# Kernel optimization log

Measured on AMD Instinct MI355X. Metric: run time of the kernel, lower is better.

The kernel has to match this reference:

```python
import jax, jax.numpy as jnp
import numpy as np

N = 100000
E = 1600000
D_IN = 128
HEADS = 4
C = 16  # hidden // heads
NEG_SLOPE = 0.2


def setup_inputs() -> dict:
    key = jax.random.key(0)
    ks = jax.random.split(key, 8)
    x = jax.random.normal(ks[0], (N, D_IN), dtype=jnp.float32)
    edge_index = jax.random.randint(ks[1], (2, E), 0, N, dtype=jnp.int32)
    s = 1.0 / np.sqrt(D_IN)
    W_l = jax.random.normal(ks[2], (D_IN, HEADS * C), dtype=jnp.float32) * s
    b_l = jnp.zeros((HEADS * C,), dtype=jnp.float32)
    W_r = jax.random.normal(ks[3], (D_IN, HEADS * C), dtype=jnp.float32) * s
    b_r = jnp.zeros((HEADS * C,), dtype=jnp.float32)
    att = jax.random.normal(ks[4], (HEADS, C), dtype=jnp.float32) * (1.0 / np.sqrt(C))
    bias = jnp.zeros((HEADS * C,), dtype=jnp.float32)
    W_head = jax.random.normal(ks[5], (HEADS * C, 1), dtype=jnp.float32) * (1.0 / np.sqrt(HEADS * C))
    b_head = jnp.zeros((1,), dtype=jnp.float32)
    return {"x": x, "edge_index": edge_index, "W_l": W_l, "b_l": b_l,
            "W_r": W_r, "b_r": b_r, "att": att, "bias": bias,
            "W_head": W_head, "b_head": b_head}


def reference(x, edge_index, W_l, b_l, W_r, b_r, att, bias, W_head, b_head):
    # GATv2Conv (PyG semantics, add_self_loops=True, concat=True)
    n = x.shape[0]
    # add self loops
    loops = jnp.arange(n, dtype=edge_index.dtype)
    src = jnp.concatenate([edge_index[0], loops])  # source j
    dst = jnp.concatenate([edge_index[1], loops])  # target i
    # per-node linear projections -> [N, H, C]
    x_l = (x @ W_l + b_l).reshape(n, HEADS, C)
    x_r = (x @ W_r + b_r).reshape(n, HEADS, C)
    # per-edge attention logits: att . LeakyReLU(x_l[j] + x_r[i])
    e = x_l[src] + x_r[dst]                               # [E', H, C]
    e = jnp.where(e >= 0, e, NEG_SLOPE * e)
    logits = jnp.einsum('ehc,hc->eh', e, att)             # [E', H]
    # segment softmax over incoming edges of each target node
    seg_max = jax.ops.segment_max(logits, dst, num_segments=n)  # [N, H]
    expw = jnp.exp(logits - seg_max[dst])
    seg_sum = jax.ops.segment_sum(expw, dst, num_segments=n)
    alpha = expw / seg_sum[dst]                           # [E', H]
    # weighted scatter-aggregate of source messages
    msg = alpha[:, :, None] * x_l[src]                    # [E', H, C]
    out = jax.ops.segment_sum(msg, dst, num_segments=n)   # [N, H, C]
    out = out.reshape(n, HEADS * C) + bias
    # ReLU + Linear head
    h = jax.nn.relu(out)
    return (h @ W_head + b_head).squeeze(-1)              # [N]
```

## Files before the change

### kernel.cpp

```cpp
#include <hip/hip_runtime.h>
#include <hip/hip_bf16.h>
#include <hip/hip_fp16.h>

#define HC 64
#define D_IN 128
#define NEG_SLOPE 0.2f
#define BK 64
#define BKQ 16
#define BCAP2 1536
#define NBIN 2048
#define L2E 1.44269504f

using f32x4 = __attribute__((ext_vector_type(4))) float;
using f16x8 = __attribute__((ext_vector_type(8))) _Float16;
using f16x2 = __attribute__((ext_vector_type(2))) _Float16;

__global__ void k_iota(int* __restrict__ p, int n) {
    int i = blockIdx.x * blockDim.x + threadIdx.x;
    if (i < n) p[i] = i * BCAP2;
}

__global__ __launch_bounds__(256, 3) void k_proj(
    const float* __restrict__ x,
    const float* __restrict__ Wl, const float* __restrict__ bl,
    const float* __restrict__ Wr, const float* __restrict__ br,
    __half* __restrict__ xlh, float* __restrict__ xr, int N) {
    __shared__ _Float16 sWT[128 * 136];
    __shared__ _Float16 sX[32 * 136];
    const int t = threadIdx.x;
    for (int idx = t; idx < 8192; idx += 256) {
        const int k = idx >> 6;
        const int c = idx & 63;
        sWT[c * 136 + k]        = (_Float16)Wl[idx];
        sWT[(c + 64) * 136 + k] = (_Float16)Wr[idx];
    }
    const int lane = t & 63;
    const int wave = t >> 6;
    const int m = lane & 15;
    const int q = lane >> 4;
    float bfu[2];
#pragma unroll
    for (int cc = 0; cc < 2; ++cc) {
        const int ct = wave * 2 + cc;
        const int ch = (ct & 3) * 16 + m;
        bfu[cc] = (ct < 4) ? bl[ch] : br[ch];
    }
    __syncthreads();

    const int ntrip = N >> 5;
    for (int trip = blockIdx.x; trip < ntrip; trip += gridDim.x) {
        const int i0 = trip << 5;
        for (int c = t; c < 1024; c += 256) {
            const int r = c >> 5, c4 = c & 31;
            float4 v = ((const float4*)(x + (size_t)(i0 + r) * D_IN))[c4];
            _Float16* dp = &sX[r * 136 + c4 * 4];
            dp[0] = (_Float16)v.x; dp[1] = (_Float16)v.y;
            dp[2] = (_Float16)v.z; dp[3] = (_Float16)v.w;
        }
        __syncthreads();
        f16x8 af[2][4];
#pragma unroll
        for (int tt = 0; tt < 2; ++tt)
#pragma unroll
            for (int kk = 0; kk < 4; ++kk)
                af[tt][kk] = *(const f16x8*)&sX[(tt * 16 + m) * 136 + kk * 32 + q * 8];
#pragma unroll
        for (int cc = 0; cc < 2; ++cc) {
            const int ct = wave * 2 + cc;
            const _Float16* bp = &sWT[(ct * 16 + m) * 136 + q * 8];
            f32x4 acc0 = {0.f, 0.f, 0.f, 0.f};
            f32x4 acc1 = {0.f, 0.f, 0.f, 0.f};
#pragma unroll
            for (int kk = 0; kk < 4; ++kk) {
                f16x8 bf = *(const f16x8*)(bp + kk * 32);
                acc0 = __builtin_amdgcn_mfma_f32_16x16x32_f16(af[0][kk], bf, acc0, 0, 0, 0);
                acc1 = __builtin_amdgcn_mfma_f32_16x16x32_f16(af[1][kk], bf, acc1, 0, 0, 0);
            }
            const float bv = bfu[cc];
            if (ct < 4) {
                const int ch = ct * 16 + m;
#pragma unroll
                for (int r = 0; r < 4; ++r) {
                    xlh[(size_t)(i0 + q * 4 + r) * HC + ch]      = __float2half(acc0[r] + bv);
                    xlh[(size_t)(i0 + 16 + q * 4 + r) * HC + ch] = __float2half(acc1[r] + bv);
                }
            } else {
                const int ch = (ct - 4) * 16 + m;
#pragma unroll
                for (int r = 0; r < 4; ++r) {
                    xr[(size_t)(i0 + q * 4 + r) * HC + ch]      = acc0[r] + bv;
                    xr[(size_t)(i0 + 16 + q * 4 + r) * HC + ch] = acc1[r] + bv;
                }
            }
        }
        __syncthreads();
    }
}

__global__ __launch_bounds__(256) void k_scat1(const int* __restrict__ src,
                                               const int* __restrict__ dst, int E,
                                               int* __restrict__ bfill,
                                               unsigned* __restrict__ coarse) {
    __shared__ int h[NBIN], bl[NBIN], cur[NBIN];
    const int t = threadIdx.x;
    for (int i = t; i < NBIN; i += 256) { h[i] = 0; cur[i] = 0; }
    __syncthreads();
    const int beg = blockIdx.x * 4096;
    int4 d4[4], s4[4];
#pragma unroll
    for (int r = 0; r < 4; ++r) {
        const int idx = beg + 4 * t + r * 1024;
        if (idx < E) {
            d4[r] = *(const int4*)(dst + idx);
            s4[r] = *(const int4*)(src + idx);
        } else { d4[r] = make_int4(-1, -1, -1, -1); }
    }
#pragma unroll
    for (int r = 0; r < 4; ++r) {
        if (d4[r].x >= 0) {
            atomicAdd(&h[d4[r].x >> 6], 1);
            atomicAdd(&h[d4[r].y >> 6], 1);
            atomicAdd(&h[d4[r].z >> 6], 1);
            atomicAdd(&h[d4[r].w >> 6], 1);
        }
    }
    __syncthreads();
    for (int i = t; i < NBIN; i += 256)
        bl[i] = h[i] ? atomicAdd(&bfill[i], h[i]) : 0;
    __syncthreads();
#pragma unroll
    for (int r = 0; r < 4; ++r) {
        if (d4[r].x >= 0) {
            const int dd[4] = {d4[r].x, d4[r].y, d4[r].z, d4[r].w};
            const int ss[4] = {s4[r].x, s4[r].y, s4[r].z, s4[r].w};
#pragma unroll
            for (int j = 0; j < 4; ++j) {
                const int bin = dd[j] >> 6;
                const int pos = atomicAdd(&cur[bin], 1);
                coarse[bl[bin] + pos] = ((unsigned)ss[j] << 6) | (unsigned)(dd[j] & 63);
            }
        }
    }
}

__device__ __forceinline__ float redpair(float v) {
    int a = __builtin_amdgcn_update_dpp(0, __float_as_int(v), 0xB1, 0xF, 0xF, true);
    return v + __int_as_float(a);
}
__device__ __forceinline__ float red8(float v) {
    int a = __builtin_amdgcn_update_dpp(0, __float_as_int(v), 0x128, 0xF, 0xF, true);
    return v + __int_as_float(a);
}

__global__ __launch_bounds__(256) void k_aggs(
    const __half* __restrict__ xlh, const float* __restrict__ xr,
    const float* __restrict__ att, const float* __restrict__ bias,
    const float* __restrict__ Wh, const float* __restrict__ bh,
    const int* __restrict__ bfill, const unsigned* __restrict__ coarse,
    float* __restrict__ out, int N) {
    __shared__ int s_src[BCAP2];
    __shared__ int s_cnt[BKQ], s_off[BKQ], s_cur[BKQ], s_scan[BKQ];
    const int t = threadIdx.x;
    const int bkt  = blockIdx.x >> 2;
    const int quad = blockIdx.x & 3;
    const int eb = bkt * BCAP2;
    const int ee = bfill[bkt];
    if (t < BKQ) { s_cnt[t] = 0; s_cur[t] = 0; }
    __syncthreads();
    unsigned er[6]; int nr = 0;
#pragma unroll
    for (int r = 0; r < 6; ++r) {
        const int idx = eb + t + r * 256;
        if (idx < ee) {
            const unsigned e = coarse[idx];
            if (((e >> 4) & 3u) == (unsigned)quad) er[nr++] = e;
        }
    }
    for (int k = 0; k < nr; ++k) atomicAdd(&s_cnt[er[k] & 15], 1);
    __syncthreads();
    if (t < BKQ) s_scan[t] = s_cnt[t];
    __syncthreads();
    for (int o = 1; o < BKQ; o <<= 1) {
        int v = (t < BKQ && t >= o) ? s_scan[t - o] : 0;
        __syncthreads();
        if (t < BKQ) s_scan[t] += v;
        __syncthreads();
    }
    if (t < BKQ) s_off[t] = s_scan[t] - s_cnt[t];
    __syncthreads();
    for (int k = 0; k < nr; ++k) {
        const int bin = er[k] & 15;
        const int pos = atomicAdd(&s_cur[bin], 1);
        s_src[s_off[bin] + pos] = (int)(er[k] >> 6);
    }
    __syncthreads();

    const int wave = t >> 6;
    const int lane = t & 63;
    const int sub  = lane & 7;
    const int slot = lane >> 3;
    const _Float16* xlhp = (const _Float16*)xlh;

    const float4 atA = *(const float4*)(att + 8 * sub);
    const float4 atB = *(const float4*)(att + 8 * sub + 4);
    f16x2 at[4];
    at[0][0] = (_Float16)(atA.x * L2E); at[0][1] = (_Float16)(atA.y * L2E);
    at[1][0] = (_Float16)(atA.z * L2E); at[1][1] = (_Float16)(atA.w * L2E);
    at[2][0] = (_Float16)(atB.x * L2E); at[2][1] = (_Float16)(atB.y * L2E);
    at[3][0] = (_Float16)(atB.z * L2E); at[3][1] = (_Float16)(atB.w * L2E);
    const f16x2 c02 = {(_Float16)NEG_SLOPE, (_Float16)NEG_SLOPE};
    const _Float16 h0 = (_Float16)0.f;
    const float4 biA = *(const float4*)(bias + 8 * sub);
    const float4 biB = *(const float4*)(bias + 8 * sub + 4);
    const float4 whA = *(const float4*)(Wh + 8 * sub);
    const float4 whB = *(const float4*)(Wh + 8 * sub + 4);
    const float bhv = bh[0];

    for (int k4 = 0; k4 < 4; ++k4) {
        const int nl = wave + 4 * k4;
        const int i = bkt * 64 + quad * 16 + nl;
        if (i >= N) continue;
        const int beg = s_off[nl];
        const int cnt = s_cnt[nl];

        const float4 xrA = *(const float4*)(xr + ((size_t)i << 6) + 8 * sub);
        const float4 xrB = *(const float4*)(xr + ((size_t)i << 6) + 8 * sub + 4);
        f16x2 xri[4];
        xri[0][0] = (_Float16)xrA.x; xri[0][1] = (_Float16)xrA.y;
        xri[1][0] = (_Float16)xrA.z; xri[1][1] = (_Float16)xrA.w;
        xri[2][0] = (_Float16)xrB.x; xri[2][1] = (_Float16)xrB.y;
        xri[3][0] = (_Float16)xrB.z; xri[3][1] = (_Float16)xrB.w;
        const uint4 xliraw = *(const uint4*)(xlhp + ((size_t)i << 6) + 8 * sub);
        f16x2 xli[4];
        xli[0] = __builtin_bit_cast(f16x2, xliraw.x);
        xli[1] = __builtin_bit_cast(f16x2, xliraw.y);
        xli[2] = __builtin_bit_cast(f16x2, xliraw.z);
        xli[3] = __builtin_bit_cast(f16x2, xliraw.w);

        float t0 = 0.f;
#pragma unroll
        for (int c = 0; c < 4; ++c) {
            f16x2 w = xli[c] + xri[c];
            w = __builtin_elementwise_max(w, w * c02);
            t0 = __builtin_amdgcn_fdot2(at[c], w, t0, false);
        }
        t0 = redpair(t0);
        const _Float16 pe0h = (slot == 0) ? (_Float16)exp2f(t0) : h0;
        const f16x2 p0A = {pe0h, h0};
        const f16x2 p0B = {h0, pe0h};
        float s = (float)pe0h;
        float a[8];
#pragma unroll
        for (int c = 0; c < 4; ++c) {
            a[2 * c]     = __builtin_amdgcn_fdot2(xli[c], p0A, 0.f, false);
            a[2 * c + 1] = __builtin_amdgcn_fdot2(xli[c], p0B, 0.f, false);
        }

        int p = 0;
#define EDGE_GROUP(JEXPR, PRED)                                              \
    {                                                                        \
        const int jj = (JEXPR);                                              \
        const uint4 raw = *(const uint4*)(xlhp + ((size_t)jj << 6) + 8 * sub);\
        f16x2 xv[4];                                                         \
        xv[0] = __builtin_bit_cast(f16x2, raw.x);                            \
        xv[1] = __builtin_bit_cast(f16x2, raw.y);                            \
        xv[2] = __builtin_bit_cast(f16x2, raw.z);                            \
        xv[3] = __builtin_bit_cast(f16x2, raw.w);                            \
        float tt = 0.f;                                                      \
        _Pragma("unroll")                                                    \
        for (int c = 0; c < 4; ++c) {                                        \
            f16x2 w = xv[c] + xri[c];                                        \
            w = __builtin_elementwise_max(w, w * c02);                       \
            tt = __builtin_amdgcn_fdot2(at[c], w, tt, false);                \
        }                                                                    \
        tt = redpair(tt);                                                    \
        const _Float16 peh = (PRED) ? (_Float16)exp2f(tt) : h0;              \
        const f16x2 pA = {peh, h0};                                          \
        const f16x2 pB = {h0, peh};                                          \
        s += (float)peh;                                                     \
        _Pragma("unroll")                                                    \
        for (int c = 0; c < 4; ++c) {                                        \
            a[2 * c]     = __builtin_amdgcn_fdot2(xv[c], pA, a[2 * c], false);\
            a[2 * c + 1] = __builtin_amdgcn_fdot2(xv[c], pB, a[2 * c + 1], false);\
        }                                                                    \
    }
        for (; p + 16 <= cnt; p += 16) {
            const int j0 = s_src[beg + p + slot];
            const int j1 = s_src[beg + p + 8 + slot];
            EDGE_GROUP(j0, true)
            EDGE_GROUP(j1, true)
        }
        if (p + 8 <= cnt) {
            const int j0 = s_src[beg + p + slot];
            EDGE_GROUP(j0, true)
            p += 8;
        }
        const int rem = cnt - p;
        if (rem > 0) {
            const int idx = p + slot;
            const int j0 = s_src[beg + ((idx < cnt) ? idx : (cnt - 1))];
            EDGE_GROUP(j0, slot < rem)
        }
#undef EDGE_GROUP

        s = red8(s);  s += __shfl_xor(s, 16);  s += __shfl_xor(s, 32);
#pragma unroll
        for (int c = 0; c < 8; ++c) {
            a[c] = red8(a[c]);
            a[c] += __shfl_xor(a[c], 16);
            a[c] += __shfl_xor(a[c], 32);
        }
        const float inv = 1.f / s;
        float y = fmaxf(a[0] * inv + biA.x, 0.f) * whA.x
                + fmaxf(a[1] * inv + biA.y, 0.f) * whA.y
                + fmaxf(a[2] * inv + biA.z, 0.f) * whA.z
                + fmaxf(a[3] * inv + biA.w, 0.f) * whA.w
                + fmaxf(a[4] * inv + biB.x, 0.f) * whB.x
                + fmaxf(a[5] * inv + biB.y, 0.f) * whB.y
                + fmaxf(a[6] * inv + biB.z, 0.f) * whB.z
                + fmaxf(a[7] * inv + biB.w, 0.f) * whB.w;
        y += __shfl_xor(y, 1);
        y += __shfl_xor(y, 2);
        y += __shfl_xor(y, 4);
        if (lane == 0) out[i] = y + bhv;
    }
}

extern "C" void kernel_launch(void* const* d_in, const int* in_sizes, int n_in,
                              void* d_out, int out_size, void* d_ws, size_t ws_size,
                              hipStream_t stream) {
    const float* x   = (const float*)d_in[0];
    const int*   ei  = (const int*)d_in[1];
    const float* Wl  = (const float*)d_in[2];
    const float* bl  = (const float*)d_in[3];
    const float* Wr  = (const float*)d_in[4];
    const float* br  = (const float*)d_in[5];
    const float* att = (const float*)d_in[6];
    const float* bias= (const float*)d_in[7];
    const float* Wh  = (const float*)d_in[8];
    const float* bh  = (const float*)d_in[9];
    float* out = (float*)d_out;

    const int N = in_sizes[0] / D_IN;
    const int E = in_sizes[1] / 2;
    const int* src = ei;
    const int* dst = ei + E;
    const int nbkt = (N + BK - 1) / BK;

    auto align = [](size_t v) { return (v + 255) & ~(size_t)255; };
    char* ws = (char*)d_ws;
    size_t off = 0;
    __half* xlh     = (__half*)(ws + off);   off = align(off + (size_t)N * HC * 2);
    float* xr       = (float*)(ws + off);    off = align(off + (size_t)N * HC * 4);
    int*   bfill    = (int*)(ws + off);      off = align(off + NBIN * 4);
    unsigned* coarse= (unsigned*)(ws + off); off = align(off + (size_t)NBIN * BCAP2 * 4);
    (void)ws_size;

    k_iota<<<8, 256, 0, stream>>>(bfill, NBIN);

    k_proj<<<1024, 256, 0, stream>>>(x, Wl, bl, Wr, br, xlh, xr, N);

    k_scat1<<<(E + 4095) / 4096, 256, 0, stream>>>(src, dst, E, bfill, coarse);

    k_aggs<<<nbkt * 4, 256, 0, stream>>>(xlh, xr, att, bias, Wh, bh,
                                         bfill, coarse, out, N);
}
```

Measured before the change: 208.2 us.

## Double-buffer x tiles in projection and shrink scatter blocks, reusing LDS histogram

In the projection kernel, the next tile of x is now prefetched into registers while the current tile is being processed. The shared-memory staging buffer is doubled so one barrier per iteration can be dropped, overlapping global loads with the MFMA work. In the scatter kernel, each block now handles 2048 edges instead of 4096, and the histogram array is zeroed and reused as the per-bin cursor, cutting LDS use and raising block count. The trade-off is more global atomics on the bin fill counters and shorter contiguous runs per bin in the coarse buffer.

```diff
diff --git a/kernel.cpp b/kernel.cpp
--- a/kernel.cpp
+++ b/kernel.cpp
@@ -26,7 +26,7 @@
     const float* __restrict__ Wr, const float* __restrict__ br,
     __half* __restrict__ xlh, float* __restrict__ xr, int N) {
     __shared__ _Float16 sWT[128 * 136];
-    __shared__ _Float16 sX[32 * 136];
+    __shared__ _Float16 sX[2][32 * 136];
     const int t = threadIdx.x;
     for (int idx = t; idx < 8192; idx += 256) {
         const int k = idx >> 6;
@@ -45,25 +45,42 @@
         const int ch = (ct & 3) * 16 + m;
         bfu[cc] = (ct < 4) ? bl[ch] : br[ch];
     }
-    __syncthreads();
 
     const int ntrip = N >> 5;
-    for (int trip = blockIdx.x; trip < ntrip; trip += gridDim.x) {
+    const int rr = t >> 5;
+    const int c4 = t & 31;
+    int trip = blockIdx.x;
+    int tb = 0;
+    float4 xv[4];
+    if (trip < ntrip) {
         const int i0 = trip << 5;
-        for (int c = t; c < 1024; c += 256) {
-            const int r = c >> 5, c4 = c & 31;
-            float4 v = ((const float4*)(x + (size_t)(i0 + r) * D_IN))[c4];
-            _Float16* dp = &sX[r * 136 + c4 * 4];
-            dp[0] = (_Float16)v.x; dp[1] = (_Float16)v.y;
-            dp[2] = (_Float16)v.z; dp[3] = (_Float16)v.w;
+#pragma unroll
+        for (int it = 0; it < 4; ++it)
+            xv[it] = *(const float4*)(x + (size_t)(i0 + rr + 8 * it) * D_IN + c4 * 4);
+    }
+    for (; trip < ntrip; trip += gridDim.x, ++tb) {
+        _Float16* sxb = &sX[tb & 1][0];
+#pragma unroll
+        for (int it = 0; it < 4; ++it) {
+            _Float16* dp = &sxb[(rr + 8 * it) * 136 + c4 * 4];
+            dp[0] = (_Float16)xv[it].x; dp[1] = (_Float16)xv[it].y;
+            dp[2] = (_Float16)xv[it].z; dp[3] = (_Float16)xv[it].w;
         }
         __syncthreads();
+        const int nxt = trip + gridDim.x;
+        if (nxt < ntrip) {
+            const int i0n = nxt << 5;
+#pragma unroll
+            for (int it = 0; it < 4; ++it)
+                xv[it] = *(const float4*)(x + (size_t)(i0n + rr + 8 * it) * D_IN + c4 * 4);
+        }
+        const int i0 = trip << 5;
         f16x8 af[2][4];
 #pragma unroll
         for (int tt = 0; tt < 2; ++tt)
 #pragma unroll
             for (int kk = 0; kk < 4; ++kk)
-                af[tt][kk] = *(const f16x8*)&sX[(tt * 16 + m) * 136 + kk * 32 + q * 8];
+                af[tt][kk] = *(const f16x8*)&sxb[(tt * 16 + m) * 136 + kk * 32 + q * 8];
 #pragma unroll
         for (int cc = 0; cc < 2; ++cc) {
             const int ct = wave * 2 + cc;
@@ -93,7 +110,6 @@
                 }
             }
         }
-        __syncthreads();
     }
 }
 
@@ -101,14 +117,14 @@
                                                const int* __restrict__ dst, int E,
                                                int* __restrict__ bfill,
                                                unsigned* __restrict__ coarse) {
-    __shared__ int h[NBIN], bl[NBIN], cur[NBIN];
+    __shared__ int h[NBIN], bl[NBIN];
     const int t = threadIdx.x;
-    for (int i = t; i < NBIN; i += 256) { h[i] = 0; cur[i] = 0; }
-    __syncthreads();
-    const int beg = blockIdx.x * 4096;
-    int4 d4[4], s4[4];
-#pragma unroll
-    for (int r = 0; r < 4; ++r) {
+    for (int i = t; i < NBIN; i += 256) h[i] = 0;
+    __syncthreads();
+    const int beg = blockIdx.x * 2048;
+    int4 d4[2], s4[2];
+#pragma unroll
+    for (int r = 0; r < 2; ++r) {
         const int idx = beg + 4 * t + r * 1024;
         if (idx < E) {
             d4[r] = *(const int4*)(dst + idx);
@@ -116,7 +132,7 @@
         } else { d4[r] = make_int4(-1, -1, -1, -1); }
     }
 #pragma unroll
-    for (int r = 0; r < 4; ++r) {
+    for (int r = 0; r < 2; ++r) {
         if (d4[r].x >= 0) {
             atomicAdd(&h[d4[r].x >> 6], 1);
             atomicAdd(&h[d4[r].y >> 6], 1);
@@ -125,18 +141,21 @@
         }
     }
     __syncthreads();
-    for (int i = t; i < NBIN; i += 256)
-        bl[i] = h[i] ? atomicAdd(&bfill[i], h[i]) : 0;
-    __syncthreads();
-#pragma unroll
-    for (int r = 0; r < 4; ++r) {
+    for (int i = t; i < NBIN; i += 256) {
+        const int hv = h[i];
+        bl[i] = hv ? atomicAdd(&bfill[i], hv) : 0;
+        h[i] = 0;
+    }
+    __syncthreads();
+#pragma unroll
+    for (int r = 0; r < 2; ++r) {
         if (d4[r].x >= 0) {
             const int dd[4] = {d4[r].x, d4[r].y, d4[r].z, d4[r].w};
             const int ss[4] = {s4[r].x, s4[r].y, s4[r].z, s4[r].w};
 #pragma unroll
             for (int j = 0; j < 4; ++j) {
                 const int bin = dd[j] >> 6;
-                const int pos = atomicAdd(&cur[bin], 1);
+                const int pos = atomicAdd(&h[bin], 1);
                 coarse[bl[bin] + pos] = ((unsigned)ss[j] << 6) | (unsigned)(dd[j] & 63);
             }
         }
@@ -360,7 +379,7 @@
 
     k_proj<<<1024, 256, 0, stream>>>(x, Wl, bl, Wr, br, xlh, xr, N);
 
-    k_scat1<<<(E + 4095) / 4096, 256, 0, stream>>>(src, dst, E, bfill, coarse);
+    k_scat1<<<(E + 2047) / 2048, 256, 0, stream>>>(src, dst, E, bfill, coarse);
 
     k_aggs<<<nbkt * 4, 256, 0, stream>>>(xlh, xr, att, bias, Wh, bh,
                                          bfill, coarse, out, N);
```

New measurement: 215.5 us. 3.5% more time.

## Keep projection weights in registers, load x directly, stage outputs for coalesced stores

Applied to the files above, without the earlier changes.

The projection kernel now keeps each wave's fp16 weight fragments in registers instead of transposing them into shared memory. It loads x straight from global memory into MFMA operand registers, skipping the shared-memory staging pass. Outputs are written to a small shared tile and then stored with coalesced 16-byte writes instead of scattered 2- and 4-byte stores. Occupancy is raised to 4 blocks per SM, at the cost of more register pressure and strided, uncoalesced reads of x and W.

```diff
diff --git a/kernel.cpp b/kernel.cpp
--- a/kernel.cpp
+++ b/kernel.cpp
@@ -20,78 +20,93 @@
     if (i < n) p[i] = i * BCAP2;
 }
 
-__global__ __launch_bounds__(256, 3) void k_proj(
+__global__ __launch_bounds__(256, 4) void k_proj(
     const float* __restrict__ x,
     const float* __restrict__ Wl, const float* __restrict__ bl,
     const float* __restrict__ Wr, const float* __restrict__ br,
     __half* __restrict__ xlh, float* __restrict__ xr, int N) {
-    __shared__ _Float16 sWT[128 * 136];
-    __shared__ _Float16 sX[32 * 136];
+    __shared__ _Float16 sH[32 * 64];
+    __shared__ float    sF[32 * 64];
     const int t = threadIdx.x;
-    for (int idx = t; idx < 8192; idx += 256) {
-        const int k = idx >> 6;
-        const int c = idx & 63;
-        sWT[c * 136 + k]        = (_Float16)Wl[idx];
-        sWT[(c + 64) * 136 + k] = (_Float16)Wr[idx];
-    }
     const int lane = t & 63;
     const int wave = t >> 6;
     const int m = lane & 15;
     const int q = lane >> 4;
+
+    f16x8 bf[2][4];
     float bfu[2];
 #pragma unroll
     for (int cc = 0; cc < 2; ++cc) {
         const int ct = wave * 2 + cc;
         const int ch = (ct & 3) * 16 + m;
+        const float* W = (ct < 4) ? Wl : Wr;
         bfu[cc] = (ct < 4) ? bl[ch] : br[ch];
-    }
-    __syncthreads();
+#pragma unroll
+        for (int kk = 0; kk < 4; ++kk) {
+            const float* wp = W + (size_t)(kk * 32 + q * 8) * 64 + ch;
+            f16x8 v;
+#pragma unroll
+            for (int e = 0; e < 8; ++e)
+                v[e] = (_Float16)wp[(size_t)e * 64];
+            bf[cc][kk] = v;
+        }
+    }
 
     const int ntrip = N >> 5;
     for (int trip = blockIdx.x; trip < ntrip; trip += gridDim.x) {
         const int i0 = trip << 5;
-        for (int c = t; c < 1024; c += 256) {
-            const int r = c >> 5, c4 = c & 31;
-            float4 v = ((const float4*)(x + (size_t)(i0 + r) * D_IN))[c4];
-            _Float16* dp = &sX[r * 136 + c4 * 4];
-            dp[0] = (_Float16)v.x; dp[1] = (_Float16)v.y;
-            dp[2] = (_Float16)v.z; dp[3] = (_Float16)v.w;
-        }
-        __syncthreads();
         f16x8 af[2][4];
 #pragma unroll
-        for (int tt = 0; tt < 2; ++tt)
-#pragma unroll
-            for (int kk = 0; kk < 4; ++kk)
-                af[tt][kk] = *(const f16x8*)&sX[(tt * 16 + m) * 136 + kk * 32 + q * 8];
+        for (int tt = 0; tt < 2; ++tt) {
+            const float* xp = x + (size_t)(i0 + tt * 16 + m) * D_IN + q * 8;
+#pragma unroll
+            for (int kk = 0; kk < 4; ++kk) {
+                const float4 f0 = *(const float4*)(xp + kk * 32);
+                const float4 f1 = *(const float4*)(xp + kk * 32 + 4);
+                f16x8 v;
+                v[0] = (_Float16)f0.x; v[1] = (_Float16)f0.y;
+                v[2] = (_Float16)f0.z; v[3] = (_Float16)f0.w;
+                v[4] = (_Float16)f1.x; v[5] = (_Float16)f1.y;
+                v[6] = (_Float16)f1.z; v[7] = (_Float16)f1.w;
+                af[tt][kk] = v;
+            }
+        }
 #pragma unroll
         for (int cc = 0; cc < 2; ++cc) {
             const int ct = wave * 2 + cc;
-            const _Float16* bp = &sWT[(ct * 16 + m) * 136 + q * 8];
             f32x4 acc0 = {0.f, 0.f, 0.f, 0.f};
             f32x4 acc1 = {0.f, 0.f, 0.f, 0.f};
 #pragma unroll
             for (int kk = 0; kk < 4; ++kk) {
-                f16x8 bf = *(const f16x8*)(bp + kk * 32);
-                acc0 = __builtin_amdgcn_mfma_f32_16x16x32_f16(af[0][kk], bf, acc0, 0, 0, 0);
-                acc1 = __builtin_amdgcn_mfma_f32_16x16x32_f16(af[1][kk], bf, acc1, 0, 0, 0);
+                acc0 = __builtin_amdgcn_mfma_f32_16x16x32_f16(af[0][kk], bf[cc][kk], acc0, 0, 0, 0);
+                acc1 = __builtin_amdgcn_mfma_f32_16x16x32_f16(af[1][kk], bf[cc][kk], acc1, 0, 0, 0);
             }
             const float bv = bfu[cc];
             if (ct < 4) {
                 const int ch = ct * 16 + m;
 #pragma unroll
                 for (int r = 0; r < 4; ++r) {
-                    xlh[(size_t)(i0 + q * 4 + r) * HC + ch]      = __float2half(acc0[r] + bv);
-                    xlh[(size_t)(i0 + 16 + q * 4 + r) * HC + ch] = __float2half(acc1[r] + bv);
+                    sH[(q * 4 + r) * 64 + ch]      = (_Float16)(acc0[r] + bv);
+                    sH[(16 + q * 4 + r) * 64 + ch] = (_Float16)(acc1[r] + bv);
                 }
             } else {
                 const int ch = (ct - 4) * 16 + m;
 #pragma unroll
                 for (int r = 0; r < 4; ++r) {
-                    xr[(size_t)(i0 + q * 4 + r) * HC + ch]      = acc0[r] + bv;
-                    xr[(size_t)(i0 + 16 + q * 4 + r) * HC + ch] = acc1[r] + bv;
+                    sF[(q * 4 + r) * 64 + ch]      = acc0[r] + bv;
+                    sF[(16 + q * 4 + r) * 64 + ch] = acc1[r] + bv;
                 }
             }
+        }
+        __syncthreads();
+        {
+            const uint4* srcH = (const uint4*)sH;
+            uint4* dstH = (uint4*)(xlh + (size_t)i0 * 64);
+            dstH[t] = srcH[t];
+            const uint4* srcF = (const uint4*)sF;
+            uint4* dstF = (uint4*)(xr + (size_t)i0 * 64);
+            dstF[t]       = srcF[t];
+            dstF[t + 256] = srcF[t + 256];
         }
         __syncthreads();
     }
```

After: 212.8 us. +2.2%, slower.

## Merge projection and edge scatter into one launch; store x_r as fp16

Applied to the files above, without the earlier changes.

The projection GEMM and the edge-bucketing scatter now run as one kernel. The first nscat blocks do the scatter and the rest run the projection loop, so the two independent phases overlap and one launch is dropped. x_r is also written as fp16 instead of fp32, which halves its write and read traffic and removes the conversion in the aggregation kernel. The cost is a shared-memory union sized for the larger branch, which may limit occupancy, plus slightly lower precision in the stored x_r.

```diff
diff --git a/kernel.cpp b/kernel.cpp
--- a/kernel.cpp
+++ b/kernel.cpp
@@ -20,14 +20,66 @@
     if (i < n) p[i] = i * BCAP2;
 }
 
-__global__ __launch_bounds__(256, 3) void k_proj(
+__global__ __launch_bounds__(256, 3) void k_projscat(
     const float* __restrict__ x,
     const float* __restrict__ Wl, const float* __restrict__ bl,
     const float* __restrict__ Wr, const float* __restrict__ br,
-    __half* __restrict__ xlh, float* __restrict__ xr, int N) {
-    __shared__ _Float16 sWT[128 * 136];
-    __shared__ _Float16 sX[32 * 136];
+    __half* __restrict__ xlh, __half* __restrict__ xrh,
+    const int* __restrict__ src, const int* __restrict__ dst, int E,
+    int* __restrict__ bfill, unsigned* __restrict__ coarse, int N) {
+    __shared__ __align__(16) char smem[43520];
     const int t = threadIdx.x;
+    const int nscat = (E + 4095) >> 12;
+
+    if ((int)blockIdx.x < nscat) {
+        int* h   = (int*)smem;
+        int* sbl = (int*)(smem + 8192);
+        int* cur = (int*)(smem + 16384);
+        for (int i = t; i < NBIN; i += 256) { h[i] = 0; cur[i] = 0; }
+        __syncthreads();
+        const int beg = blockIdx.x * 4096;
+        int4 d4[4], s4[4];
+#pragma unroll
+        for (int r = 0; r < 4; ++r) {
+            const int idx = beg + 4 * t + r * 1024;
+            if (idx < E) {
+                d4[r] = *(const int4*)(dst + idx);
+                s4[r] = *(const int4*)(src + idx);
+            } else { d4[r] = make_int4(-1, -1, -1, -1); }
+        }
+#pragma unroll
+        for (int r = 0; r < 4; ++r) {
+            if (d4[r].x >= 0) {
+                atomicAdd(&h[d4[r].x >> 6], 1);
+                atomicAdd(&h[d4[r].y >> 6], 1);
+                atomicAdd(&h[d4[r].z >> 6], 1);
+                atomicAdd(&h[d4[r].w >> 6], 1);
+            }
+        }
+        __syncthreads();
+        for (int i = t; i < NBIN; i += 256)
+            sbl[i] = h[i] ? atomicAdd(&bfill[i], h[i]) : 0;
+        __syncthreads();
+#pragma unroll
+        for (int r = 0; r < 4; ++r) {
+            if (d4[r].x >= 0) {
+                const int dd[4] = {d4[r].x, d4[r].y, d4[r].z, d4[r].w};
+                const int ss[4] = {s4[r].x, s4[r].y, s4[r].z, s4[r].w};
+#pragma unroll
+                for (int j = 0; j < 4; ++j) {
+                    const int bin = dd[j] >> 6;
+                    const int pos = atomicAdd(&cur[bin], 1);
+                    coarse[sbl[bin] + pos] = ((unsigned)ss[j] << 6) | (unsigned)(dd[j] & 63);
+                }
+            }
+        }
+        return;
+    }
+
+    _Float16* sWT = (_Float16*)smem;
+    _Float16* sX  = (_Float16*)(smem + 34816);
+    const int pb  = blockIdx.x - nscat;
+    const int npb = gridDim.x - nscat;
     for (int idx = t; idx < 8192; idx += 256) {
         const int k = idx >> 6;
         const int c = idx & 63;
@@ -48,7 +100,7 @@
     __syncthreads();
 
     const int ntrip = N >> 5;
-    for (int trip = blockIdx.x; trip < ntrip; trip += gridDim.x) {
+    for (int trip = pb; trip < ntrip; trip += npb) {
         const int i0 = trip << 5;
         for (int c = t; c < 1024; c += 256) {
             const int r = c >> 5, c4 = c & 31;
@@ -77,69 +129,15 @@
                 acc1 = __builtin_amdgcn_mfma_f32_16x16x32_f16(af[1][kk], bf, acc1, 0, 0, 0);
             }
             const float bv = bfu[cc];
-            if (ct < 4) {
-                const int ch = ct * 16 + m;
-#pragma unroll
-                for (int r = 0; r < 4; ++r) {
-                    xlh[(size_t)(i0 + q * 4 + r) * HC + ch]      = __float2half(acc0[r] + bv);
-                    xlh[(size_t)(i0 + 16 + q * 4 + r) * HC + ch] = __float2half(acc1[r] + bv);
-                }
-            } else {
-                const int ch = (ct - 4) * 16 + m;
-#pragma unroll
-                for (int r = 0; r < 4; ++r) {
-                    xr[(size_t)(i0 + q * 4 + r) * HC + ch]      = acc0[r] + bv;
-                    xr[(size_t)(i0 + 16 + q * 4 + r) * HC + ch] = acc1[r] + bv;
-                }
+            __half* dstA = (ct < 4) ? xlh : xrh;
+            const int ch = (ct & 3) * 16 + m;
+#pragma unroll
+            for (int r = 0; r < 4; ++r) {
+                dstA[(size_t)(i0 + q * 4 + r) * HC + ch]      = __float2half(acc0[r] + bv);
+                dstA[(size_t)(i0 + 16 + q * 4 + r) * HC + ch] = __float2half(acc1[r] + bv);
             }
         }
         __syncthreads();
-    }
-}
-
-__global__ __launch_bounds__(256) void k_scat1(const int* __restrict__ src,
-                                               const int* __restrict__ dst, int E,
-                                               int* __restrict__ bfill,
-                                               unsigned* __restrict__ coarse) {
-    __shared__ int h[NBIN], bl[NBIN], cur[NBIN];
-    const int t = threadIdx.x;
-    for (int i = t; i < NBIN; i += 256) { h[i] = 0; cur[i] = 0; }
-    __syncthreads();
-    const int beg = blockIdx.x * 4096;
-    int4 d4[4], s4[4];
-#pragma unroll
-    for (int r = 0; r < 4; ++r) {
-        const int idx = beg + 4 * t + r * 1024;
-        if (idx < E) {
-            d4[r] = *(const int4*)(dst + idx);
-            s4[r] = *(const int4*)(src + idx);
-        } else { d4[r] = make_int4(-1, -1, -1, -1); }
-    }
-#pragma unroll
-    for (int r = 0; r < 4; ++r) {
-        if (d4[r].x >= 0) {
-            atomicAdd(&h[d4[r].x >> 6], 1);
-            atomicAdd(&h[d4[r].y >> 6], 1);
-            atomicAdd(&h[d4[r].z >> 6], 1);
-            atomicAdd(&h[d4[r].w >> 6], 1);
-        }
-    }
-    __syncthreads();
-    for (int i = t; i < NBIN; i += 256)
-        bl[i] = h[i] ? atomicAdd(&bfill[i], h[i]) : 0;
-    __syncthreads();
-#pragma unroll
-    for (int r = 0; r < 4; ++r) {
-        if (d4[r].x >= 0) {
-            const int dd[4] = {d4[r].x, d4[r].y, d4[r].z, d4[r].w};
-            const int ss[4] = {s4[r].x, s4[r].y, s4[r].z, s4[r].w};
-#pragma unroll
-            for (int j = 0; j < 4; ++j) {
-                const int bin = dd[j] >> 6;
-                const int pos = atomicAdd(&cur[bin], 1);
-                coarse[bl[bin] + pos] = ((unsigned)ss[j] << 6) | (unsigned)(dd[j] & 63);
-            }
-        }
     }
 }
 
@@ -153,7 +151,7 @@
 }
 
 __global__ __launch_bounds__(256) void k_aggs(
-    const __half* __restrict__ xlh, const float* __restrict__ xr,
+    const __half* __restrict__ xlh, const __half* __restrict__ xrh,
     const float* __restrict__ att, const float* __restrict__ bias,
     const float* __restrict__ Wh, const float* __restrict__ bh,
     const int* __restrict__ bfill, const unsigned* __restrict__ coarse,
@@ -200,6 +198,7 @@
     const int sub  = lane & 7;
     const int slot = lane >> 3;
     const _Float16* xlhp = (const _Float16*)xlh;
+    const _Float16* xrhp = (const _Float16*)xrh;
 
     const float4 atA = *(const float4*)(att + 8 * sub);
     const float4 atB = *(const float4*)(att + 8 * sub + 4);
@@ -223,15 +222,13 @@
         const int beg = s_off[nl];
         const int cnt = s_cnt[nl];
 
-        const float4 xrA = *(const float4*)(xr + ((size_t)i << 6) + 8 * sub);
-        const float4 xrB = *(const float4*)(xr + ((size_t)i << 6) + 8 * sub + 4);
-        f16x2 xri[4];
-        xri[0][0] = (_Float16)xrA.x; xri[0][1] = (_Float16)xrA.y;
-        xri[1][0] = (_Float16)xrA.z; xri[1][1] = (_Float16)xrA.w;
-        xri[2][0] = (_Float16)xrB.x; xri[2][1] = (_Float16)xrB.y;
-        xri[3][0] = (_Float16)xrB.z; xri[3][1] = (_Float16)xrB.w;
+        const uint4 xrraw = *(const uint4*)(xrhp + ((size_t)i << 6) + 8 * sub);
         const uint4 xliraw = *(const uint4*)(xlhp + ((size_t)i << 6) + 8 * sub);
-        f16x2 xli[4];
+        f16x2 xri[4], xli[4];
+        xri[0] = __builtin_bit_cast(f16x2, xrraw.x);
+        xri[1] = __builtin_bit_cast(f16x2, xrraw.y);
+        xri[2] = __builtin_bit_cast(f16x2, xrraw.z);
+        xri[3] = __builtin_bit_cast(f16x2, xrraw.w);
         xli[0] = __builtin_bit_cast(f16x2, xliraw.x);
         xli[1] = __builtin_bit_cast(f16x2, xliraw.y);
         xli[2] = __builtin_bit_cast(f16x2, xliraw.z);
@@ -346,22 +343,22 @@
     const int* src = ei;
     const int* dst = ei + E;
     const int nbkt = (N + BK - 1) / BK;
+    const int nscat = (E + 4095) / 4096;
 
     auto align = [](size_t v) { return (v + 255) & ~(size_t)255; };
     char* ws = (char*)d_ws;
     size_t off = 0;
     __half* xlh     = (__half*)(ws + off);   off = align(off + (size_t)N * HC * 2);
-    float* xr       = (float*)(ws + off);    off = align(off + (size_t)N * HC * 4);
+    __half* xrh     = (__half*)(ws + off);   off = align(off + (size_t)N * HC * 2);
     int*   bfill    = (int*)(ws + off);      off = align(off + NBIN * 4);
     unsigned* coarse= (unsigned*)(ws + off); off = align(off + (size_t)NBIN * BCAP2 * 4);
     (void)ws_size;
 
     k_iota<<<8, 256, 0, stream>>>(bfill, NBIN);
 
-    k_proj<<<1024, 256, 0, stream>>>(x, Wl, bl, Wr, br, xlh, xr, N);
-
-    k_scat1<<<(E + 4095) / 4096, 256, 0, stream>>>(src, dst, E, bfill, coarse);
-
-    k_aggs<<<nbkt * 4, 256, 0, stream>>>(xlh, xr, att, bias, Wh, bh,
+    k_projscat<<<nscat + 1024, 256, 0, stream>>>(x, Wl, bl, Wr, br, xlh, xrh,
+                                                 src, dst, E, bfill, coarse, N);
+
+    k_aggs<<<nbkt * 4, 256, 0, stream>>>(xlh, xrh, att, bias, Wh, bh,
                                          bfill, coarse, out, N);
 }
```

New measurement: 201.7 us. 3.1% less time.
